# Performance work log

Measured on AMD Instinct MI355X. Metric: run time of the kernel, lower is better.

Reference implementation:

```python
import jax, jax.numpy as jnp
import numpy as np

B, C_IN, H, W = 8, 128, 64, 64
C_KEY, C_VAL, C_OUT = 64, 64, 128
BN_EPS = 1e-5
NORM_EPS = 1e-7


def setup_inputs() -> dict:
    key = jax.random.key(0)
    ks = jax.random.split(key, 8)
    s = 0.02
    return {
        "query_feature": jax.random.normal(ks[0], (B, C_IN, H, W), jnp.float32),
        "key_feature": jax.random.normal(ks[1], (B, C_IN, H, W), jnp.float32),
        "value_feature": jax.random.normal(ks[2], (B, C_IN, H, W), jnp.float32),
        "Wk": jax.random.normal(ks[3], (C_KEY, C_IN), jnp.float32) * s,  # shared f_key/f_query 1x1 conv
        "bk": jnp.zeros((C_KEY,), jnp.float32),
        "gamma": jnp.ones((C_KEY,), jnp.float32),   # BatchNorm2d weight
        "beta": jnp.zeros((C_KEY,), jnp.float32),   # BatchNorm2d bias
        "Wv": jax.random.normal(ks[4], (C_VAL, C_IN), jnp.float32) * s,
        "bv": jnp.zeros((C_VAL,), jnp.float32),
        "Ww": jax.random.normal(ks[5], (C_OUT, C_VAL), jnp.float32) * s,  # zero-init in original; random for nontrivial output
        "bw": jnp.zeros((C_OUT,), jnp.float32),
    }


def _conv1x1(x, w, b):
    # x: [B,C,H,W], w: [O,C] -> [B,O,H,W]
    return jnp.einsum('bchw,oc->bohw', x, w) + b[None, :, None, None]


def _bn_train(y, gamma, beta):
    # BatchNorm2d in train mode: batch stats over (B,H,W) per channel
    m = y.mean(axis=(0, 2, 3), keepdims=True)
    v = y.var(axis=(0, 2, 3), keepdims=True)
    return (y - m) * jax.lax.rsqrt(v + BN_EPS) * gamma[None, :, None, None] + beta[None, :, None, None]


def reference(query_feature, key_feature, value_feature, Wk, bk, gamma, beta, Wv, bv, Ww, bw):
    b, _, h, w = query_feature.shape
    n = h * w

    def f_key(x):
        return _bn_train(_conv1x1(x, Wk, bk), gamma, beta)

    # query: [B,N,Ck], key: [B,Ck,N], value: [B,N,Cv]
    q = f_key(query_feature).reshape(b, C_KEY, n).transpose(0, 2, 1)
    k = f_key(key_feature).reshape(b, C_KEY, n)
    v = _conv1x1(value_feature, Wv, bv).reshape(b, C_VAL, n).transpose(0, 2, 1)

    # L2-normalize over channel dim (cosine similarity)
    q = q / (jnp.linalg.norm(q, axis=2, keepdims=True) + NORM_EPS)
    k = k / (jnp.linalg.norm(k, axis=1, keepdims=True) + NORM_EPS)

    sim = jnp.einsum('bnc,bcm->bnm', q, k) + 1.0     # [B,N,N], no softmax
    ctx = jnp.einsum('bnm,bmv->bnv', sim, v)         # [B,N,Cv]
    ctx = ctx.transpose(0, 2, 1).reshape(b, C_VAL, h, w)
    return _conv1x1(ctx, Ww, bw)
```

## Files before the change

kernel.cpp:

```cpp
#include <hip/hip_runtime.h>
#include <math.h>

#define NTOT 4096
#define NBATCH 8
#define CIN 128
#define CK 64
#define CV 64
#define CO 128
#define BN_COUNT 32768.0f

#define OFF_YQ    0ul
#define OFF_YK    2097152ul
#define OFF_V     4194304ul
#define OFF_STATS 6291456ul
#define OFF_VSUM  6293504ul
#define OFF_MP    2097152ul
#define OFF_DP    2228224ul

__global__ __launch_bounds__(256) void gemm3_kernel(
    const float* __restrict__ Xq, const float* __restrict__ Xk, const float* __restrict__ Xv,
    const float* __restrict__ Wk, const float* __restrict__ bk,
    const float* __restrict__ Wv, const float* __restrict__ bv,
    float* __restrict__ Yq, float* __restrict__ Yk, float* __restrict__ Vv)
{
    const int chunk = blockIdx.x;
    const int b     = blockIdx.y;
    const int which = blockIdx.z;
    const float* X    = (which == 0) ? Xq : (which == 1) ? Xk : Xv;
    const float* W    = (which == 2) ? Wv : Wk;
    const float* bias = (which == 2) ? bv : bk;
    float* Y          = (which == 0) ? Yq : (which == 1) ? Yk : Vv;

    __shared__ float sX[CIN][64];

    const int t = threadIdx.x;
    const int lane = t & 63;
    const int wu = __builtin_amdgcn_readfirstlane(t >> 6);

    const int n0 = chunk * 64;
    const float* Xb = X + (size_t)b * (CIN * NTOT) + n0;

#pragma unroll
    for (int r = 0; r < 8; ++r) {
        int idx4 = t + r * 256;
        int c  = idx4 >> 4;
        int j4 = (idx4 & 15) << 2;
        float4 xv = *(const float4*)(Xb + (size_t)c * NTOT + j4);
        *(float4*)&sX[c][j4] = xv;
    }
    __syncthreads();

    const float* Wp = W + (size_t)wu * 16 * CIN;
    float acc[16];
#pragma unroll
    for (int ki = 0; ki < 16; ++ki) acc[ki] = 0.f;

#pragma unroll 8
    for (int c = 0; c < CIN; ++c) {
        float xv = sX[c][lane];
#pragma unroll
        for (int ki = 0; ki < 16; ++ki)
            acc[ki] += xv * Wp[ki * CIN + c];
    }

    float* Yb = Y + (size_t)b * (CK * NTOT) + n0;
#pragma unroll
    for (int ki = 0; ki < 16; ++ki) {
        int o = wu * 16 + ki;
        Yb[(size_t)o * NTOT + lane] = acc[ki] + bias[o];
    }
}

__global__ __launch_bounds__(256) void stats_kernel(
    const float* __restrict__ Yq, const float* __restrict__ Yk,
    float* __restrict__ stats)
{
    const int nsplit = blockIdx.x;
    const int c      = blockIdx.y;
    const int which  = blockIdx.z;
    const float* Y = which ? Yk : Yq;
    const int t = threadIdx.x;

    float s = 0.f, ss = 0.f;
#pragma unroll
    for (int p = 0; p < 4; ++p) {
        int b = (t >> 7) + p * 2;
        int e = (t & 127) << 2;
        const float* src = Y + (size_t)b * (CK * NTOT) + (size_t)c * NTOT
                         + nsplit * 512 + e;
        float4 v = *(const float4*)src;
        s  += v.x + v.y + v.z + v.w;
        ss += v.x * v.x + v.y * v.y + v.z * v.z + v.w * v.w;
    }
#pragma unroll
    for (int off = 32; off > 0; off >>= 1) {
        s  += __shfl_down(s, off, 64);
        ss += __shfl_down(ss, off, 64);
    }
    __shared__ float red[8];
    int wave = t >> 6, lane = t & 63;
    if (lane == 0) { red[wave * 2] = s; red[wave * 2 + 1] = ss; }
    __syncthreads();
    if (t == 0) {
        float S  = red[0] + red[2] + red[4] + red[6];
        float SS = red[1] + red[3] + red[5] + red[7];
        atomicAdd(&stats[(which * 64 + c) * 16],     S);
        atomicAdd(&stats[(which * 64 + c) * 16 + 4], SS);
    }
}

__global__ __launch_bounds__(256) void kv_kernel(
    const float* __restrict__ Yk, const float* __restrict__ Vv,
    const float* __restrict__ stats, const float* __restrict__ gamma,
    const float* __restrict__ beta, float* __restrict__ KVp,
    float* __restrict__ vsum)
{
    const int chunk = blockIdx.x;
    const int b     = blockIdx.y;
    __shared__ float sk[64][68];
    __shared__ float sv[64][68];
    __shared__ float pn[4][64];
    __shared__ float rn[64];
    __shared__ float sscl[64], sshf[64];

    const int t = threadIdx.x;
    const int wave = t >> 6, lane = t & 63;
    if (t < 64) {
        float S  = stats[(64 + t) * 16];
        float SS = stats[(64 + t) * 16 + 4];
        float mean = S * (1.f / BN_COUNT);
        float var  = SS * (1.f / BN_COUNT) - mean * mean;
        float scl  = gamma[t] * rsqrtf(var + 1e-5f);
        sscl[t] = scl;
        sshf[t] = beta[t] - mean * scl;
    }
    __syncthreads();

    const int n0 = chunk * 64;
    const float* Ykb = Yk + (size_t)b * (CK * NTOT) + n0;
    const float* Vb  = Vv + (size_t)b * (CK * NTOT) + n0;

#pragma unroll
    for (int r = 0; r < 4; ++r) {
        int idx4 = t + r * 256;
        int c  = idx4 >> 4;
        int j4 = (idx4 & 15) << 2;
        float4 kf = *(const float4*)(Ykb + (size_t)c * NTOT + j4);
        float4 vf = *(const float4*)(Vb  + (size_t)c * NTOT + j4);
        float scl = sscl[c], sh = sshf[c];
        float4 ks = make_float4(kf.x * scl + sh, kf.y * scl + sh,
                                kf.z * scl + sh, kf.w * scl + sh);
        *(float4*)&sk[c][j4] = ks;
        *(float4*)&sv[c][j4] = vf;
    }
    __syncthreads();

    {
        float s = 0.f;
#pragma unroll
        for (int i = 0; i < 16; ++i) { float x = sk[wave * 16 + i][lane]; s += x * x; }
        pn[wave][lane] = s;
    }
    {
        const int v = t >> 2, q = t & 3;
        float s = 0.f;
#pragma unroll
        for (int i = 0; i < 16; ++i) s += sv[v][q * 16 + i];
        s += __shfl_down(s, 2, 64);
        s += __shfl_down(s, 1, 64);
        if (q == 0) atomicAdd(&vsum[((size_t)b * 64 + v) * 16], s);
    }
    __syncthreads();
    if (t < 64)
        rn[t] = 1.f / (sqrtf(pn[0][t] + pn[1][t] + pn[2][t] + pn[3][t]) + 1e-7f);
    __syncthreads();

    const int tc = t >> 4, tv = t & 15;
    float acc[4][4];
#pragma unroll
    for (int i = 0; i < 4; ++i)
#pragma unroll
        for (int k2 = 0; k2 < 4; ++k2) acc[i][k2] = 0.f;

#pragma unroll 2
    for (int jq = 0; jq < 16; ++jq) {
        float4 rq = *(const float4*)&rn[jq * 4];
        float4 a4[4], b4[4];
#pragma unroll
        for (int i = 0; i < 4; ++i) {
            float4 k4 = *(const float4*)&sk[tc * 4 + i][jq * 4];
            a4[i] = make_float4(k4.x * rq.x, k4.y * rq.y, k4.z * rq.z, k4.w * rq.w);
        }
#pragma unroll
        for (int k2 = 0; k2 < 4; ++k2) b4[k2] = *(const float4*)&sv[tv * 4 + k2][jq * 4];
#pragma unroll
        for (int i = 0; i < 4; ++i)
#pragma unroll
            for (int k2 = 0; k2 < 4; ++k2) {
                acc[i][k2] += a4[i].x * b4[k2].x + a4[i].y * b4[k2].y
                            + a4[i].z * b4[k2].z + a4[i].w * b4[k2].w;
            }
    }

    float* P = KVp + ((size_t)(b * 64 + chunk)) * 4096;
#pragma unroll
    for (int i = 0; i < 4; ++i) {
        float4 st = make_float4(acc[i][0], acc[i][1], acc[i][2], acc[i][3]);
        *(float4*)&P[(tc * 4 + i) * 64 + tv * 4] = st;
    }
}

__global__ __launch_bounds__(256) void m_kernel(
    const float* __restrict__ KVp, const float* __restrict__ vsum,
    const float* __restrict__ Ww, const float* __restrict__ bw,
    float* __restrict__ Mp, float* __restrict__ dp)
{
    const int half = blockIdx.x;
    const int b    = blockIdx.y;
    __shared__ float sKV[64][36];
    __shared__ float sWw[128][36];
    __shared__ float svs[32];
    const int t = threadIdx.x;

#pragma unroll
    for (int r = 0; r < 4; ++r) {
        int idx4 = t + r * 256;
        int o  = idx4 >> 3;
        int v4 = (idx4 & 7) << 2;
        *(float4*)&sWw[o][v4] = *(const float4*)(Ww + (size_t)o * 64 + half * 32 + v4);
    }
    if (t < 32) svs[t] = vsum[((size_t)b * 64 + half * 32 + t) * 16];

    const float* base = KVp + (size_t)b * 64 * 4096;
    const int c0  = t >> 3;
    const int vq0 = (t & 7) << 2;
    const size_t off0 = (size_t)c0 * 64 + half * 32 + vq0;
    const size_t off1 = (size_t)(c0 + 32) * 64 + half * 32 + vq0;
    float4 r0 = make_float4(0.f, 0.f, 0.f, 0.f);
    float4 r1 = make_float4(0.f, 0.f, 0.f, 0.f);
#pragma unroll 4
    for (int ch = 0; ch < 64; ++ch) {
        const float* pc = base + (size_t)ch * 4096;
        float4 x0 = *(const float4*)(pc + off0);
        float4 x1 = *(const float4*)(pc + off1);
        r0.x += x0.x; r0.y += x0.y; r0.z += x0.z; r0.w += x0.w;
        r1.x += x1.x; r1.y += x1.y; r1.z += x1.z; r1.w += x1.w;
    }
    *(float4*)&sKV[c0][vq0]      = r0;
    *(float4*)&sKV[c0 + 32][vq0] = r1;
    __syncthreads();

    const int c  = t & 63;
    const int og = (t >> 6) * 32;
    float kreg[32];
#pragma unroll
    for (int vq = 0; vq < 8; ++vq) {
        float4 kv4 = *(const float4*)&sKV[c][vq * 4];
        kreg[vq * 4 + 0] = kv4.x; kreg[vq * 4 + 1] = kv4.y;
        kreg[vq * 4 + 2] = kv4.z; kreg[vq * 4 + 3] = kv4.w;
    }
    float* Mpb = Mp + ((size_t)b * 2 + half) * 8192;
#pragma unroll
    for (int oi = 0; oi < 32; ++oi) {
        const int o = og + oi;
        float acc = 0.f;
#pragma unroll
        for (int vq = 0; vq < 8; ++vq) {
            float4 w4 = *(const float4*)&sWw[o][vq * 4];
            acc += kreg[vq * 4 + 0] * w4.x + kreg[vq * 4 + 1] * w4.y
                 + kreg[vq * 4 + 2] * w4.z + kreg[vq * 4 + 3] * w4.w;
        }
        Mpb[(size_t)c * CO + o] = acc;
    }

    if (t < 128) {
        float acc = (half == 0) ? bw[t] : 0.f;
#pragma unroll 8
        for (int v = 0; v < 32; ++v) acc += sWw[t][v] * svs[v];
        dp[((size_t)b * 2 + half) * 128 + t] = acc;
    }
}

__global__ __launch_bounds__(256) void out_kernel(
    const float* __restrict__ Yq, const float* __restrict__ stats,
    const float* __restrict__ gamma, const float* __restrict__ beta,
    const float* __restrict__ Mp, const float* __restrict__ dp,
    float* __restrict__ out)
{
    const int chunk = blockIdx.x;
    const int b     = blockIdx.y;
    __shared__ float sM[CK * CO];
    __shared__ float sq[64][68];
    __shared__ float pn[4][64];
    __shared__ float rn[64];
    __shared__ float sd[CO];
    __shared__ float sscl[64], sshf[64];

    const int t = threadIdx.x;
    const int wave = t >> 6, lane = t & 63;
    const int n0 = chunk * 64;

    const float* Mp0 = Mp + (size_t)b * 2 * 8192;
    const float* Mp1 = Mp0 + 8192;
#pragma unroll
    for (int r = 0; r < 8; ++r) {
        int idx4 = t + r * 256;
        float4 m0 = ((const float4*)Mp0)[idx4];
        float4 m1 = ((const float4*)Mp1)[idx4];
        ((float4*)sM)[idx4] = make_float4(m0.x + m1.x, m0.y + m1.y,
                                          m0.z + m1.z, m0.w + m1.w);
    }
    if (t < CO) sd[t] = dp[(size_t)b * 2 * 128 + t] + dp[((size_t)b * 2 + 1) * 128 + t];
    if (t < 64) {
        float S  = stats[t * 16];
        float SS = stats[t * 16 + 4];
        float mean = S * (1.f / BN_COUNT);
        float var  = SS * (1.f / BN_COUNT) - mean * mean;
        float scl  = gamma[t] * rsqrtf(var + 1e-5f);
        sscl[t] = scl;
        sshf[t] = beta[t] - mean * scl;
    }
    __syncthreads();

    const float* Yb = Yq + (size_t)b * (CK * NTOT) + n0;
#pragma unroll
    for (int r = 0; r < 4; ++r) {
        int idx4 = t + r * 256;
        int c  = idx4 >> 4;
        int j4 = (idx4 & 15) << 2;
        float4 xv = *(const float4*)(Yb + (size_t)c * NTOT + j4);
        float scl = sscl[c], sh = sshf[c];
        sq[c][j4 + 0] = xv.x * scl + sh;
        sq[c][j4 + 1] = xv.y * scl + sh;
        sq[c][j4 + 2] = xv.z * scl + sh;
        sq[c][j4 + 3] = xv.w * scl + sh;
    }
    __syncthreads();

    {
        float s = 0.f;
#pragma unroll
        for (int i = 0; i < 16; ++i) { float x = sq[wave * 16 + i][lane]; s += x * x; }
        pn[wave][lane] = s;
    }
    __syncthreads();
    if (t < 64)
        rn[t] = 1.f / (sqrtf(pn[0][t] + pn[1][t] + pn[2][t] + pn[3][t]) + 1e-7f);
    __syncthreads();

    const int j0 = (t & 15) << 2;
    const int o0 = (t >> 4) << 3;
    float acc[4][8];
#pragma unroll
    for (int jj = 0; jj < 4; ++jj)
#pragma unroll
        for (int oo = 0; oo < 8; ++oo) acc[jj][oo] = 0.f;

#pragma unroll 4
    for (int c = 0; c < 64; ++c) {
        float4 qv = *(const float4*)&sq[c][j0];
        float4 m0 = *(const float4*)&sM[c * CO + o0];
        float4 m1 = *(const float4*)&sM[c * CO + o0 + 4];
        float aq[4] = {qv.x, qv.y, qv.z, qv.w};
        float am[8] = {m0.x, m0.y, m0.z, m0.w, m1.x, m1.y, m1.z, m1.w};
#pragma unroll
        for (int jj = 0; jj < 4; ++jj)
#pragma unroll
            for (int oo = 0; oo < 8; ++oo) acc[jj][oo] += aq[jj] * am[oo];
    }

    float4 rq = *(const float4*)&rn[j0];
    float rnj[4] = {rq.x, rq.y, rq.z, rq.w};

    float* outb = out + (size_t)b * (CO * NTOT) + n0;
#pragma unroll
    for (int oo = 0; oo < 8; ++oo) {
        float dd = sd[o0 + oo];
        float4 st = make_float4(acc[0][oo] * rnj[0] + dd,
                                acc[1][oo] * rnj[1] + dd,
                                acc[2][oo] * rnj[2] + dd,
                                acc[3][oo] * rnj[3] + dd);
        *(float4*)&outb[(size_t)(o0 + oo) * NTOT + j0] = st;
    }
}

extern "C" void kernel_launch(void* const* d_in, const int* in_sizes, int n_in,
                              void* d_out, int out_size, void* d_ws, size_t ws_size,
                              hipStream_t stream) {
    (void)in_sizes; (void)n_in; (void)out_size; (void)ws_size;
    const float* q     = (const float*)d_in[0];
    const float* k     = (const float*)d_in[1];
    const float* v     = (const float*)d_in[2];
    const float* Wk    = (const float*)d_in[3];
    const float* bk    = (const float*)d_in[4];
    const float* gamma = (const float*)d_in[5];
    const float* beta  = (const float*)d_in[6];
    const float* Wv    = (const float*)d_in[7];
    const float* bv    = (const float*)d_in[8];
    const float* Ww    = (const float*)d_in[9];
    const float* bw    = (const float*)d_in[10];
    float* out = (float*)d_out;
    float* ws  = (float*)d_ws;

    float* Yq    = ws + OFF_YQ;
    float* Yk    = ws + OFF_YK;
    float* Vv    = ws + OFF_V;
    float* stats = ws + OFF_STATS;
    float* vsum  = ws + OFF_VSUM;
    float* Mp    = ws + OFF_MP;
    float* dp    = ws + OFF_DP;
    float* KVp   = out;

    hipMemsetAsync(stats, 0, (2048 + 8192) * sizeof(float), stream);

    gemm3_kernel<<<dim3(64, NBATCH, 3), 256, 0, stream>>>(
        q, k, v, Wk, bk, Wv, bv, Yq, Yk, Vv);
    stats_kernel<<<dim3(8, 64, 2), 256, 0, stream>>>(Yq, Yk, stats);
    kv_kernel<<<dim3(64, NBATCH), 256, 0, stream>>>(Yk, Vv, stats, gamma, beta, KVp, vsum);
    m_kernel<<<dim3(2, NBATCH), 256, 0, stream>>>(KVp, vsum, Ww, bw, Mp, dp);
    out_kernel<<<dim3(64, NBATCH), 256, 0, stream>>>(Yq, stats, gamma, beta, Mp, dp, out);
}
```

Before: 189.3 us.

## Split M reduction across channel slices and halve out_kernel tile width

m_kernel now launches 16 slices per batch, each reducing the partial KV sums for 4 key channels over all 64 value channels. It writes the final M and d directly instead of two half-partials that out_kernel had to add. out_kernel processes 32 spatial positions per block with 1024 blocks instead of 64 positions with 512, using a smaller per-thread register tile. The goal is more parallelism in the formerly 16-block reduction kernel and higher occupancy in the output stage. The cost is that each out_kernel block still reloads the full 32KB M matrix, now twice as often in total.

```diff
diff --git a/kernel.cpp b/kernel.cpp
--- a/kernel.cpp
+++ b/kernel.cpp
@@ -14,8 +14,8 @@
 #define OFF_V     4194304ul
 #define OFF_STATS 6291456ul
 #define OFF_VSUM  6293504ul
-#define OFF_MP    2097152ul
-#define OFF_DP    2228224ul
+#define OFF_M     2097152ul
+#define OFF_D     2162688ul
 
 __global__ __launch_bounds__(256) void gemm3_kernel(
     const float* __restrict__ Xq, const float* __restrict__ Xk, const float* __restrict__ Xv,
@@ -213,104 +213,96 @@
 __global__ __launch_bounds__(256) void m_kernel(
     const float* __restrict__ KVp, const float* __restrict__ vsum,
     const float* __restrict__ Ww, const float* __restrict__ bw,
-    float* __restrict__ Mp, float* __restrict__ dp)
+    float* __restrict__ M, float* __restrict__ d)
 {
-    const int half = blockIdx.x;
-    const int b    = blockIdx.y;
-    __shared__ float sKV[64][36];
-    __shared__ float sWw[128][36];
-    __shared__ float svs[32];
+    const int slice = blockIdx.x;
+    const int b     = blockIdx.y;
+    __shared__ float part[256][4];
+    __shared__ float sKV[4][68];
+    __shared__ float sWw[128][68];
+    __shared__ float svs[64];
     const int t = threadIdx.x;
 
 #pragma unroll
-    for (int r = 0; r < 4; ++r) {
+    for (int r = 0; r < 8; ++r) {
         int idx4 = t + r * 256;
-        int o  = idx4 >> 3;
-        int v4 = (idx4 & 7) << 2;
-        *(float4*)&sWw[o][v4] = *(const float4*)(Ww + (size_t)o * 64 + half * 32 + v4);
-    }
-    if (t < 32) svs[t] = vsum[((size_t)b * 64 + half * 32 + t) * 16];
-
-    const float* base = KVp + (size_t)b * 64 * 4096;
-    const int c0  = t >> 3;
-    const int vq0 = (t & 7) << 2;
-    const size_t off0 = (size_t)c0 * 64 + half * 32 + vq0;
-    const size_t off1 = (size_t)(c0 + 32) * 64 + half * 32 + vq0;
-    float4 r0 = make_float4(0.f, 0.f, 0.f, 0.f);
-    float4 r1 = make_float4(0.f, 0.f, 0.f, 0.f);
+        int o  = idx4 >> 4;
+        int v4 = (idx4 & 15) << 2;
+        *(float4*)&sWw[o][v4] = *(const float4*)(Ww + (size_t)o * 64 + v4);
+    }
+    if (t < 64) svs[t] = vsum[((size_t)b * 64 + t) * 16];
+
+    const int chl = t >> 6;
+    const int ci  = (t >> 4) & 3;
+    const int v4  = (t & 15) << 2;
+    const size_t rowoff = ((size_t)(slice * 4 + ci)) * 64 + v4;
+    float4 a4 = make_float4(0.f, 0.f, 0.f, 0.f);
 #pragma unroll 4
-    for (int ch = 0; ch < 64; ++ch) {
-        const float* pc = base + (size_t)ch * 4096;
-        float4 x0 = *(const float4*)(pc + off0);
-        float4 x1 = *(const float4*)(pc + off1);
-        r0.x += x0.x; r0.y += x0.y; r0.z += x0.z; r0.w += x0.w;
-        r1.x += x1.x; r1.y += x1.y; r1.z += x1.z; r1.w += x1.w;
-    }
-    *(float4*)&sKV[c0][vq0]      = r0;
-    *(float4*)&sKV[c0 + 32][vq0] = r1;
-    __syncthreads();
-
-    const int c  = t & 63;
-    const int og = (t >> 6) * 32;
-    float kreg[32];
-#pragma unroll
-    for (int vq = 0; vq < 8; ++vq) {
-        float4 kv4 = *(const float4*)&sKV[c][vq * 4];
-        kreg[vq * 4 + 0] = kv4.x; kreg[vq * 4 + 1] = kv4.y;
-        kreg[vq * 4 + 2] = kv4.z; kreg[vq * 4 + 3] = kv4.w;
-    }
-    float* Mpb = Mp + ((size_t)b * 2 + half) * 8192;
-#pragma unroll
-    for (int oi = 0; oi < 32; ++oi) {
-        const int o = og + oi;
+    for (int it = 0; it < 16; ++it) {
+        int ch = it * 4 + chl;
+        float4 x = *(const float4*)(KVp + ((size_t)(b * 64 + ch)) * 4096 + rowoff);
+        a4.x += x.x; a4.y += x.y; a4.z += x.z; a4.w += x.w;
+    }
+    *(float4*)&part[t][0] = a4;
+    __syncthreads();
+    if (t < 64) {
+        float4 p0 = *(const float4*)&part[t][0];
+        float4 p1 = *(const float4*)&part[t + 64][0];
+        float4 p2 = *(const float4*)&part[t + 128][0];
+        float4 p3 = *(const float4*)&part[t + 192][0];
+        *(float4*)&sKV[(t >> 4) & 3][(t & 15) << 2] =
+            make_float4(p0.x + p1.x + p2.x + p3.x, p0.y + p1.y + p2.y + p3.y,
+                        p0.z + p1.z + p2.z + p3.z, p0.w + p1.w + p2.w + p3.w);
+    }
+    __syncthreads();
+
+    float* Mb = M + (size_t)b * (CK * CO);
+#pragma unroll
+    for (int rep = 0; rep < 2; ++rep) {
+        int idx = t + rep * 256;
+        int c = idx >> 7, o = idx & 127;
         float acc = 0.f;
 #pragma unroll
-        for (int vq = 0; vq < 8; ++vq) {
-            float4 w4 = *(const float4*)&sWw[o][vq * 4];
-            acc += kreg[vq * 4 + 0] * w4.x + kreg[vq * 4 + 1] * w4.y
-                 + kreg[vq * 4 + 2] * w4.z + kreg[vq * 4 + 3] * w4.w;
+        for (int vq = 0; vq < 16; ++vq) {
+            float4 kv4 = *(const float4*)&sKV[c][vq * 4];
+            float4 w4  = *(const float4*)&sWw[o][vq * 4];
+            acc += kv4.x * w4.x + kv4.y * w4.y + kv4.z * w4.z + kv4.w * w4.w;
         }
-        Mpb[(size_t)c * CO + o] = acc;
-    }
-
-    if (t < 128) {
-        float acc = (half == 0) ? bw[t] : 0.f;
-#pragma unroll 8
-        for (int v = 0; v < 32; ++v) acc += sWw[t][v] * svs[v];
-        dp[((size_t)b * 2 + half) * 128 + t] = acc;
+        Mb[(size_t)(slice * 4 + c) * CO + o] = acc;
+    }
+
+    if (slice == 0 && t < 128) {
+        float acc = bw[t];
+#pragma unroll 16
+        for (int v = 0; v < 64; ++v) acc += sWw[t][v] * svs[v];
+        d[(size_t)b * CO + t] = acc;
     }
 }
 
 __global__ __launch_bounds__(256) void out_kernel(
     const float* __restrict__ Yq, const float* __restrict__ stats,
     const float* __restrict__ gamma, const float* __restrict__ beta,
-    const float* __restrict__ Mp, const float* __restrict__ dp,
+    const float* __restrict__ M, const float* __restrict__ d,
     float* __restrict__ out)
 {
     const int chunk = blockIdx.x;
     const int b     = blockIdx.y;
     __shared__ float sM[CK * CO];
-    __shared__ float sq[64][68];
-    __shared__ float pn[4][64];
-    __shared__ float rn[64];
+    __shared__ float sq[64][36];
+    __shared__ float pn[8][32];
+    __shared__ float rn[32];
     __shared__ float sd[CO];
     __shared__ float sscl[64], sshf[64];
 
     const int t = threadIdx.x;
-    const int wave = t >> 6, lane = t & 63;
-    const int n0 = chunk * 64;
-
-    const float* Mp0 = Mp + (size_t)b * 2 * 8192;
-    const float* Mp1 = Mp0 + 8192;
+    const int n0 = chunk * 32;
+
 #pragma unroll
     for (int r = 0; r < 8; ++r) {
         int idx4 = t + r * 256;
-        float4 m0 = ((const float4*)Mp0)[idx4];
-        float4 m1 = ((const float4*)Mp1)[idx4];
-        ((float4*)sM)[idx4] = make_float4(m0.x + m1.x, m0.y + m1.y,
-                                          m0.z + m1.z, m0.w + m1.w);
-    }
-    if (t < CO) sd[t] = dp[(size_t)b * 2 * 128 + t] + dp[((size_t)b * 2 + 1) * 128 + t];
+        ((float4*)sM)[idx4] = ((const float4*)(M + (size_t)b * (CK * CO)))[idx4];
+    }
+    if (t < CO) sd[t] = d[(size_t)b * CO + t];
     if (t < 64) {
         float S  = stats[t * 16];
         float SS = stats[t * 16 + 4];
@@ -324,10 +316,10 @@
 
     const float* Yb = Yq + (size_t)b * (CK * NTOT) + n0;
 #pragma unroll
-    for (int r = 0; r < 4; ++r) {
+    for (int r = 0; r < 2; ++r) {
         int idx4 = t + r * 256;
-        int c  = idx4 >> 4;
-        int j4 = (idx4 & 15) << 2;
+        int c  = idx4 >> 3;
+        int j4 = (idx4 & 7) << 2;
         float4 xv = *(const float4*)(Yb + (size_t)c * NTOT + j4);
         float scl = sscl[c], sh = sshf[c];
         sq[c][j4 + 0] = xv.x * scl + sh;
@@ -338,48 +330,50 @@
     __syncthreads();
 
     {
+        const int col = t & 31, g = t >> 5;
         float s = 0.f;
 #pragma unroll
-        for (int i = 0; i < 16; ++i) { float x = sq[wave * 16 + i][lane]; s += x * x; }
-        pn[wave][lane] = s;
-    }
-    __syncthreads();
-    if (t < 64)
-        rn[t] = 1.f / (sqrtf(pn[0][t] + pn[1][t] + pn[2][t] + pn[3][t]) + 1e-7f);
-    __syncthreads();
-
-    const int j0 = (t & 15) << 2;
-    const int o0 = (t >> 4) << 3;
-    float acc[4][8];
+        for (int i = 0; i < 8; ++i) { float x = sq[g * 8 + i][col]; s += x * x; }
+        pn[g][col] = s;
+    }
+    __syncthreads();
+    if (t < 32) {
+        float s2 = pn[0][t] + pn[1][t] + pn[2][t] + pn[3][t]
+                 + pn[4][t] + pn[5][t] + pn[6][t] + pn[7][t];
+        rn[t] = 1.f / (sqrtf(s2) + 1e-7f);
+    }
+    __syncthreads();
+
+    const int j0 = (t & 7) << 2;
+    const int o0 = (t >> 3) << 2;
+    float acc[4][4];
 #pragma unroll
     for (int jj = 0; jj < 4; ++jj)
 #pragma unroll
-        for (int oo = 0; oo < 8; ++oo) acc[jj][oo] = 0.f;
+        for (int oo = 0; oo < 4; ++oo) acc[jj][oo] = 0.f;
 
 #pragma unroll 4
     for (int c = 0; c < 64; ++c) {
         float4 qv = *(const float4*)&sq[c][j0];
         float4 m0 = *(const float4*)&sM[c * CO + o0];
-        float4 m1 = *(const float4*)&sM[c * CO + o0 + 4];
         float aq[4] = {qv.x, qv.y, qv.z, qv.w};
-        float am[8] = {m0.x, m0.y, m0.z, m0.w, m1.x, m1.y, m1.z, m1.w};
+        float am[4] = {m0.x, m0.y, m0.z, m0.w};
 #pragma unroll
         for (int jj = 0; jj < 4; ++jj)
 #pragma unroll
-            for (int oo = 0; oo < 8; ++oo) acc[jj][oo] += aq[jj] * am[oo];
+            for (int oo = 0; oo < 4; ++oo) acc[jj][oo] += aq[jj] * am[oo];
     }
 
     float4 rq = *(const float4*)&rn[j0];
-    float rnj[4] = {rq.x, rq.y, rq.z, rq.w};
 
     float* outb = out + (size_t)b * (CO * NTOT) + n0;
 #pragma unroll
-    for (int oo = 0; oo < 8; ++oo) {
+    for (int oo = 0; oo < 4; ++oo) {
         float dd = sd[o0 + oo];
-        float4 st = make_float4(acc[0][oo] * rnj[0] + dd,
-                                acc[1][oo] * rnj[1] + dd,
-                                acc[2][oo] * rnj[2] + dd,
-                                acc[3][oo] * rnj[3] + dd);
+        float4 st = make_float4(acc[0][oo] * rq.x + dd,
+                                acc[1][oo] * rq.y + dd,
+                                acc[2][oo] * rq.z + dd,
+                                acc[3][oo] * rq.w + dd);
         *(float4*)&outb[(size_t)(o0 + oo) * NTOT + j0] = st;
     }
 }
@@ -407,8 +401,8 @@
     float* Vv    = ws + OFF_V;
     float* stats = ws + OFF_STATS;
     float* vsum  = ws + OFF_VSUM;
-    float* Mp    = ws + OFF_MP;
-    float* dp    = ws + OFF_DP;
+    float* M     = ws + OFF_M;
+    float* dd    = ws + OFF_D;
     float* KVp   = out;
 
     hipMemsetAsync(stats, 0, (2048 + 8192) * sizeof(float), stream);
@@ -417,6 +411,6 @@
         q, k, v, Wk, bk, Wv, bv, Yq, Yk, Vv);
     stats_kernel<<<dim3(8, 64, 2), 256, 0, stream>>>(Yq, Yk, stats);
     kv_kernel<<<dim3(64, NBATCH), 256, 0, stream>>>(Yk, Vv, stats, gamma, beta, KVp, vsum);
-    m_kernel<<<dim3(2, NBATCH), 256, 0, stream>>>(KVp, vsum, Ww, bw, Mp, dp);
-    out_kernel<<<dim3(64, NBATCH), 256, 0, stream>>>(Yq, stats, gamma, beta, Mp, dp, out);
-}
+    m_kernel<<<dim3(16, NBATCH), 256, 0, stream>>>(KVp, vsum, Ww, bw, M, dd);
+    out_kernel<<<dim3(128, NBATCH), 256, 0, stream>>>(Yq, stats, gamma, beta, M, dd, out);
+}
```

New measurement: 180.7 us. -4.6%, faster.
